# Kernel tuning notes

Measured on AMD Instinct MI355X. Metric: run time of the kernel, lower is better.

Reference implementation:

```python
import jax, jax.numpy as jnp
import numpy as np

B, S, D = 2, 2048, 1024
H, HD = 16, 64  # num_heads, head_dim
EPS = 1e-6      # flax LayerNorm default
ROPE_BASE = 10000.0


def _layernorm(x, scale, bias=None, eps=EPS):
    mu = jnp.mean(x, axis=-1, keepdims=True)
    var = jnp.mean(jnp.square(x - mu), axis=-1, keepdims=True)
    y = (x - mu) * jax.lax.rsqrt(var + eps) * scale
    return y + bias if bias is not None else y


def _rotate_half(x):
    x1, x2 = x[..., : x.shape[-1] // 2], x[..., x.shape[-1] // 2 :]
    return jnp.concatenate((-x2, x1), axis=-1)


def _rope_tables(seq_len, head_dim, dtype):
    inv_freq = 1.0 / ROPE_BASE ** (jnp.arange(0, head_dim, 2, dtype=jnp.float32) / head_dim)
    t = jnp.arange(seq_len, dtype=jnp.float32)
    freqs = jnp.einsum('i,j->ij', t, inv_freq)          # [S, HD/2]
    emb = jnp.concatenate((freqs, freqs), axis=-1)      # [S, HD]
    return jnp.cos(emb).astype(dtype), jnp.sin(emb).astype(dtype)


def setup_inputs() -> dict:
    key = jax.random.key(0)
    ks = jax.random.split(key, 4)
    return {
        'x': jax.random.normal(ks[0], (B, S, D), dtype=jnp.float32),
        'w_qkv': jax.random.normal(ks[1], (D, 3 * D), dtype=jnp.float32) * (1.0 / np.sqrt(D)),
        'b_qkv': jnp.zeros((3 * D,), dtype=jnp.float32),
        'w_out': jax.random.normal(ks[2], (D, D), dtype=jnp.float32) * (0.1 / np.sqrt(D)),
        'b_out': jnp.zeros((D,), dtype=jnp.float32),
        'ln_scale': jnp.ones((D,), dtype=jnp.float32),
        'ln_bias': jnp.zeros((D,), dtype=jnp.float32),
        'q_scale': jnp.ones((HD,), dtype=jnp.float32),
        'k_scale': jnp.ones((HD,), dtype=jnp.float32),
    }


def reference(x, w_qkv, b_qkv, w_out, b_out, ln_scale, ln_bias, q_scale, k_scale):
    b, s, d = x.shape
    # input LayerNorm
    xn = _layernorm(x, ln_scale, ln_bias)
    # fused QKV projection
    qkv = xn @ w_qkv + b_qkv                              # [B, S, 3D]
    q, k, v = jnp.split(qkv, 3, axis=-1)
    def to_bhsd(t):
        return t.reshape(b, s, H, HD).transpose(0, 2, 1, 3)
    q, k, v = to_bhsd(q), to_bhsd(k), to_bhsd(v)          # [B, H, S, HD]
    # per-head QK LayerNorm (no bias)
    q = _layernorm(q, q_scale)
    k = _layernorm(k, k_scale)
    # RoPE
    cos, sin = _rope_tables(s, HD, q.dtype)               # [S, HD]
    cos, sin = cos[None, None], sin[None, None]
    q = q * cos + _rotate_half(q) * sin
    k = k * cos + _rotate_half(k) * sin
    # scaled dot-product attention (softmax over key positions)
    scale = 1.0 / np.sqrt(HD)
    scores = jnp.einsum('bhqd,bhkd->bhqk', q, k) * scale  # [B, H, S, S]
    probs = jax.nn.softmax(scores, axis=-1)
    attn = jnp.einsum('bhqk,bhkd->bhqd', probs, v)        # [B, H, S, HD]
    attn = attn.transpose(0, 2, 1, 3).reshape(b, s, d)
    return attn @ w_out + b_out
```

## Files before the change

kernel.cpp:

```cpp
#include <hip/hip_runtime.h>
#include <math.h>

#define BB 2
#define SS 2048
#define DD 1024
#define HH 16
#define HDD 64
static constexpr float EPS = 1e-6f;

typedef __bf16 bf16x8 __attribute__((ext_vector_type(8)));
typedef __bf16 bf16x4 __attribute__((ext_vector_type(4)));
typedef float f32x4 __attribute__((ext_vector_type(4)));
typedef __attribute__((address_space(1))) const unsigned int gas_u32;
typedef __attribute__((address_space(3))) unsigned int las_u32;

__device__ __forceinline__ unsigned short f2bf(float f) {
    unsigned int u = __float_as_uint(f);
    u = (u + 0x7FFFu + ((u >> 16) & 1u)) >> 16;
    return (unsigned short)u;
}

__device__ __forceinline__ uint2 pack4bf(float a, float b, float c, float d) {
    bf16x4 v;
    v[0] = (__bf16)a; v[1] = (__bf16)b; v[2] = (__bf16)c; v[3] = (__bf16)d;
    return *(uint2*)&v;
}

__device__ __forceinline__ void async_ld16(const unsigned short* g, unsigned short* l) {
    __builtin_amdgcn_global_load_lds((gas_u32*)g, (las_u32*)l, 16, 0, 0);
}

__global__ __launch_bounds__(256) void cast_transpose(const float* __restrict__ w,
                                                      unsigned short* __restrict__ wt,
                                                      int K, int N) {
    __shared__ float tile[32][36];
    const int n0 = blockIdx.x * 32;
    const int k0 = blockIdx.y * 32;
    const int t = threadIdx.x;
    const int r = t >> 3;
    const int c = (t & 7) * 4;
    *(float4*)&tile[r][c] = *(const float4*)(w + (size_t)(k0 + r) * N + n0 + c);
    __syncthreads();
    unsigned short o[4];
#pragma unroll
    for (int i = 0; i < 4; i++) o[i] = f2bf(tile[c + i][r]);
    *(uint2*)(wt + (size_t)(n0 + r) * K + k0 + c) = *(uint2*)o;
}

__global__ __launch_bounds__(256) void rope_tables(float* __restrict__ ctab,
                                                   float* __restrict__ stab) {
    const int idx = blockIdx.x * 256 + threadIdx.x;
    const int s = idx >> 5;
    const int i = idx & 31;
    const float ang = (float)s * exp2f(-(float)i * (13.287712379549449f / 32.f));
    ctab[idx] = cosf(ang);
    stab[idx] = sinf(ang);
}

__global__ __launch_bounds__(256) void ln_kernel(const float* __restrict__ x,
                                                 const float* __restrict__ scale,
                                                 const float* __restrict__ bias,
                                                 unsigned short* __restrict__ xn) {
    __shared__ float red[4];
    const int row = blockIdx.x;
    const int t = threadIdx.x;
    const float* xr = x + (size_t)row * DD + t * 4;

    float4 v = *(const float4*)xr;
    float s = v.x + v.y + v.z + v.w;
#pragma unroll
    for (int o = 32; o; o >>= 1) s += __shfl_xor(s, o);
    if ((t & 63) == 0) red[t >> 6] = s;
    __syncthreads();
    const float mu = (red[0] + red[1] + red[2] + red[3]) * (1.f / DD);

    float4 d = {v.x - mu, v.y - mu, v.z - mu, v.w - mu};
    float sq = d.x * d.x + d.y * d.y + d.z * d.z + d.w * d.w;
#pragma unroll
    for (int o = 32; o; o >>= 1) sq += __shfl_xor(sq, o);
    __syncthreads();
    if ((t & 63) == 0) red[t >> 6] = sq;
    __syncthreads();
    const float var = (red[0] + red[1] + red[2] + red[3]) * (1.f / DD);
    const float rstd = rsqrtf(var + EPS);

    const float4 sc = *(const float4*)(scale + t * 4);
    const float4 bi = *(const float4*)(bias + t * 4);
    unsigned short o[4];
    o[0] = f2bf(d.x * rstd * sc.x + bi.x);
    o[1] = f2bf(d.y * rstd * sc.y + bi.y);
    o[2] = f2bf(d.z * rstd * sc.z + bi.z);
    o[3] = f2bf(d.w * rstd * sc.w + bi.w);
    *(uint2*)(xn + (size_t)row * DD + t * 4) = *(uint2*)o;
}

__global__ __launch_bounds__(256) void gemm_mfma_bt(const unsigned short* __restrict__ A,
                                                    const unsigned short* __restrict__ Bt,
                                                    const float* __restrict__ bias,
                                                    float* __restrict__ C,
                                                    int M, int N, int K) {
    __shared__ __align__(16) unsigned short As[128][32];
    __shared__ __align__(16) unsigned short Bs[128][32];

    const int bm = blockIdx.y * 128;
    const int bn = blockIdx.x * 128;
    const int t = threadIdx.x;
    const int wv = t >> 6;
    const int ln = t & 63;
    const int m16 = ln & 15;
    const int quad = ln >> 4;
    const int wm = (wv >> 1) * 64;
    const int wn = (wv & 1) * 64;

    f32x4 acc[4][4];
#pragma unroll
    for (int i = 0; i < 4; i++)
#pragma unroll
        for (int j = 0; j < 4; j++) acc[i][j] = (f32x4){0.f, 0.f, 0.f, 0.f};

    const int srow = wv * 32 + (ln >> 2);
    const int sk = (ln & 3) * 8;
    const unsigned short* aptr = A + (size_t)(bm + srow) * K + sk;
    const unsigned short* bptr = Bt + (size_t)(bn + srow) * K + sk;
    unsigned short* al0 = &As[wv * 32][0];
    unsigned short* al1 = &As[wv * 32 + 16][0];
    unsigned short* bl0 = &Bs[wv * 32][0];
    unsigned short* bl1 = &Bs[wv * 32 + 16][0];

    for (int k0 = 0; k0 < K; k0 += 32) {
        __syncthreads();
        async_ld16(aptr, al0);
        async_ld16(aptr + 16 * (size_t)K, al1);
        async_ld16(bptr, bl0);
        async_ld16(bptr + 16 * (size_t)K, bl1);
        __syncthreads();

        bf16x8 af[4], bf[4];
#pragma unroll
        for (int i = 0; i < 4; i++)
            af[i] = *(const bf16x8*)&As[wm + i * 16 + m16][quad * 8];
#pragma unroll
        for (int j = 0; j < 4; j++)
            bf[j] = *(const bf16x8*)&Bs[wn + j * 16 + m16][quad * 8];
#pragma unroll
        for (int i = 0; i < 4; i++)
#pragma unroll
            for (int j = 0; j < 4; j++)
                acc[i][j] = __builtin_amdgcn_mfma_f32_16x16x32_bf16(af[i], bf[j], acc[i][j], 0, 0, 0);

        aptr += 32;
        bptr += 32;
    }

#pragma unroll
    for (int j = 0; j < 4; j++) {
        const int n = bn + wn + j * 16 + m16;
        const float bv = bias[n];
#pragma unroll
        for (int i = 0; i < 4; i++) {
            float* cp = C + (size_t)(bm + wm + i * 16 + quad * 4) * N + n;
#pragma unroll
            for (int r = 0; r < 4; r++)
                cp[(size_t)r * N] = acc[i][j][r] + bv;
        }
    }
}

__global__ __launch_bounds__(256) void gemm_qkv_fused(const unsigned short* __restrict__ A,
                                                      const unsigned short* __restrict__ Bt,
                                                      const float* __restrict__ bias,
                                                      const float* __restrict__ q_scale,
                                                      const float* __restrict__ k_scale,
                                                      const float* __restrict__ ctab,
                                                      const float* __restrict__ stab,
                                                      unsigned short* __restrict__ qt,
                                                      unsigned short* __restrict__ kt,
                                                      unsigned short* __restrict__ vt,
                                                      int K) {
    __shared__ __align__(16) unsigned short As[128][32];
    __shared__ __align__(16) unsigned short Bs[128][32];

    const int bm = blockIdx.y * 128;
    const int bn = blockIdx.x * 128;
    const int t = threadIdx.x;
    const int wv = t >> 6;
    const int ln = t & 63;
    const int m16 = ln & 15;
    const int quad = ln >> 4;
    const int wm = (wv >> 1) * 64;
    const int wn = (wv & 1) * 64;

    f32x4 acc[4][4];
#pragma unroll
    for (int i = 0; i < 4; i++)
#pragma unroll
        for (int j = 0; j < 4; j++) acc[i][j] = (f32x4){0.f, 0.f, 0.f, 0.f};

    const int srow = wv * 32 + (ln >> 2);
    const int sk = (ln & 3) * 8;
    const unsigned short* aptr = A + (size_t)(bm + srow) * K + sk;
    const unsigned short* bptr = Bt + (size_t)(bn + srow) * K + sk;
    unsigned short* al0 = &As[wv * 32][0];
    unsigned short* al1 = &As[wv * 32 + 16][0];
    unsigned short* bl0 = &Bs[wv * 32][0];
    unsigned short* bl1 = &Bs[wv * 32 + 16][0];

    for (int k0 = 0; k0 < K; k0 += 32) {
        __syncthreads();
        async_ld16(aptr, al0);
        async_ld16(aptr + 16 * (size_t)K, al1);
        async_ld16(bptr, bl0);
        async_ld16(bptr + 16 * (size_t)K, bl1);
        __syncthreads();

        bf16x8 af[4], bf[4];
#pragma unroll
        for (int i = 0; i < 4; i++)
            af[i] = *(const bf16x8*)&As[wm + i * 16 + m16][quad * 8];
#pragma unroll
        for (int j = 0; j < 4; j++)
            bf[j] = *(const bf16x8*)&Bs[wn + j * 16 + m16][quad * 8];
#pragma unroll
        for (int i = 0; i < 4; i++)
#pragma unroll
            for (int j = 0; j < 4; j++)
                acc[i][j] = __builtin_amdgcn_mfma_f32_16x16x32_bf16(af[i], bf[j], acc[i][j], 0, 0, 0);

        aptr += 32;
        bptr += 32;
    }

    const int type = bn >> 10;
    const int h = ((bn & 1023) + wn) >> 6;
    const int rowbase = bm + wm;

    if (type == 2) {
        float bv[4];
#pragma unroll
        for (int j = 0; j < 4; j++) bv[j] = bias[bn + wn + j * 16 + m16];
#pragma unroll
        for (int i = 0; i < 4; i++) {
#pragma unroll
            for (int r = 0; r < 4; r++) {
                const int R = rowbase + i * 16 + quad * 4 + r;
                const int b_ = R >> 11;
                const int s_ = R & (SS - 1);
                unsigned short* orow =
                    vt + (((size_t)(b_ * HH + h) * SS) + s_) * HDD + m16;
#pragma unroll
                for (int j = 0; j < 4; j++)
                    orow[j * 16] = f2bf(acc[i][j][r] + bv[j]);
            }
        }
    } else {
        const float* scalp = (type == 0) ? q_scale : k_scale;
        const float outscale = (type == 0) ? 0.18033688011112042f : 1.0f;
        unsigned short* dst = (type == 0) ? qt : kt;
        float scl[4], bv[4];
#pragma unroll
        for (int j = 0; j < 4; j++) {
            scl[j] = scalp[j * 16 + m16];
            bv[j] = bias[bn + wn + j * 16 + m16];
        }
#pragma unroll
        for (int i = 0; i < 4; i++) {
#pragma unroll
            for (int r = 0; r < 4; r++) {
                const int R = rowbase + i * 16 + quad * 4 + r;
                const int b_ = R >> 11;
                const int s_ = R & (SS - 1);
                float v0 = acc[i][0][r] + bv[0];
                float v1 = acc[i][1][r] + bv[1];
                float v2 = acc[i][2][r] + bv[2];
                float v3 = acc[i][3][r] + bv[3];
                float sm = v0 + v1 + v2 + v3;
                sm += __shfl_xor(sm, 1);
                sm += __shfl_xor(sm, 2);
                sm += __shfl_xor(sm, 4);
                sm += __shfl_xor(sm, 8);
                const float mu = sm * (1.f / 64.f);
                v0 -= mu; v1 -= mu; v2 -= mu; v3 -= mu;
                float sq = v0 * v0 + v1 * v1 + v2 * v2 + v3 * v3;
                sq += __shfl_xor(sq, 1);
                sq += __shfl_xor(sq, 2);
                sq += __shfl_xor(sq, 4);
                sq += __shfl_xor(sq, 8);
                const float rstd = rsqrtf(sq * (1.f / 64.f) + EPS);
                v0 *= rstd * scl[0];
                v1 *= rstd * scl[1];
                v2 *= rstd * scl[2];
                v3 *= rstd * scl[3];
                const float c0 = ctab[s_ * 32 + m16];
                const float s0 = stab[s_ * 32 + m16];
                const float c1 = ctab[s_ * 32 + 16 + m16];
                const float s1 = stab[s_ * 32 + 16 + m16];
                const float o0 = (v0 * c0 - v2 * s0) * outscale;
                const float o1 = (v1 * c1 - v3 * s1) * outscale;
                const float o2 = (v2 * c0 + v0 * s0) * outscale;
                const float o3 = (v3 * c1 + v1 * s1) * outscale;
                unsigned short* orow =
                    dst + (((size_t)(b_ * HH + h) * SS) + s_) * HDD + m16;
                orow[0]  = f2bf(o0);
                orow[16] = f2bf(o1);
                orow[32] = f2bf(o2);
                orow[48] = f2bf(o3);
            }
        }
    }
}

__global__ __launch_bounds__(256) void transpose_v(const unsigned short* __restrict__ vt,
                                                   unsigned short* __restrict__ vtT) {
    __shared__ unsigned short tile[64][72];
    const int bh = blockIdx.x >> 5;
    const int s0 = (blockIdx.x & 31) * 64;
    const int t = threadIdx.x;
    const int row = t >> 2;
    const int c0 = (t & 3) * 16;
    const unsigned short* src = vt + ((size_t)bh * SS + s0 + row) * HDD + c0;
    *(uint4*)&tile[row][c0]     = *(const uint4*)(src);
    *(uint4*)&tile[row][c0 + 8] = *(const uint4*)(src + 8);
    __syncthreads();
    unsigned short outv[16];
#pragma unroll
    for (int i = 0; i < 16; i++) outv[i] = tile[c0 + i][row];
    unsigned short* dst = vtT + ((size_t)bh * HDD + row) * SS + s0 + c0;
    *(uint4*)dst       = *(uint4*)&outv[0];
    *(uint4*)(dst + 8) = *(uint4*)&outv[8];
}

__global__ __launch_bounds__(256, 4) void attn_mfma(const unsigned short* __restrict__ qt,
                                                    const unsigned short* __restrict__ kt,
                                                    const unsigned short* __restrict__ vtT,
                                                    unsigned short* __restrict__ attn) {
    __shared__ __align__(16) unsigned short KsS[64 * 64];
    __shared__ __align__(16) unsigned short VsS[64 * 64];
    __shared__ __align__(16) unsigned short PbS[4][16 * 64];

    const int bid = blockIdx.x;
    const int swz = (bid & 7) * 128 + (bid >> 3);
    const int bh = swz >> 5;
    const int q0 = (swz & 31) * 64;
    const int t = threadIdx.x;
    const int wq = t >> 6;
    const int lane = t & 63;
    const int m16 = lane & 15;
    const int quad = lane >> 4;
    const int m7 = m16 & 7;

    const int cs = quad ^ m7;
    const int koff = m16 * 64 + cs * 8;
    const int srow = t >> 2;
    const int sch = (t & 3) * 2;
    const int sw0 = srow * 64 + ((sch)     ^ (srow & 7)) * 8;
    const int sw1 = srow * 64 + ((sch + 1) ^ (srow & 7)) * 8;
    const int pwb = m16 * 64 + 4 * (quad & 1);
    const int qh = quad >> 1;

    bf16x8 qb[2];
    {
        const unsigned short* qp =
            qt + ((size_t)bh * SS + q0 + wq * 16 + m16) * HDD + quad * 8;
        qb[0] = *(const bf16x8*)qp;
        qb[1] = *(const bf16x8*)(qp + 32);
    }

    bf16x8 ones;
#pragma unroll
    for (int j = 0; j < 8; j++) ones[j] = (__bf16)1.0f;

    f32x4 O[4];
#pragma unroll
    for (int f = 0; f < 4; f++) O[f] = (f32x4){0.f, 0.f, 0.f, 0.f};
    f32x4 lacc = (f32x4){0.f, 0.f, 0.f, 0.f};

    const unsigned short* kbase = kt + (size_t)bh * SS * HDD;
    const unsigned short* vbase = vtT + (size_t)bh * HDD * SS;
    const f32x4 cinit = (f32x4){-12.f, -12.f, -12.f, -12.f};

    uint4 kr0, kr1, vr0, vr1;
    {
        const unsigned short* ksrc = kbase + (size_t)srow * HDD + sch * 8;
        const unsigned short* vsrc = vbase + (size_t)srow * SS + sch * 8;
        kr0 = *(const uint4*)ksrc;
        kr1 = *(const uint4*)(ksrc + 8);
        vr0 = *(const uint4*)vsrc;
        vr1 = *(const uint4*)(vsrc + 8);
    }

    for (int k0 = 0; k0 < SS; k0 += 64) {
        __syncthreads();
        *(uint4*)&KsS[sw0] = kr0;
        *(uint4*)&KsS[sw1] = kr1;
        *(uint4*)&VsS[sw0] = vr0;
        *(uint4*)&VsS[sw1] = vr1;
        __syncthreads();

        f32x4 S[4];
        __builtin_amdgcn_s_setprio(1);
#pragma unroll
        for (int g = 0; g < 4; g++) {
            const bf16x8 ka0 = *(const bf16x8*)&KsS[g * 1024 + koff];
            const bf16x8 ka1 = *(const bf16x8*)&KsS[g * 1024 + (koff ^ 32)];
            f32x4 a = __builtin_amdgcn_mfma_f32_16x16x32_bf16(ka0, qb[0], cinit, 0, 0, 0);
            a = __builtin_amdgcn_mfma_f32_16x16x32_bf16(ka1, qb[1], a, 0, 0, 0);
            S[g] = a;
        }
        __builtin_amdgcn_s_setprio(0);

#pragma unroll
        for (int g = 0; g < 4; g++) {
            const float p0 = exp2f(S[g][0]);
            const float p1 = exp2f(S[g][1]);
            const float p2 = exp2f(S[g][2]);
            const float p3 = exp2f(S[g][3]);
            *(uint2*)&PbS[wq][pwb + ((2 * g + qh) ^ m7) * 8] =
                pack4bf(p0, p1, p2, p3);
        }

        if (k0 + 64 < SS) {
            const unsigned short* ksrc = kbase + (size_t)(k0 + 64 + srow) * HDD + sch * 8;
            const unsigned short* vsrc = vbase + (size_t)srow * SS + (k0 + 64) + sch * 8;
            kr0 = *(const uint4*)ksrc;
            kr1 = *(const uint4*)(ksrc + 8);
            vr0 = *(const uint4*)vsrc;
            vr1 = *(const uint4*)(vsrc + 8);
        }

        asm volatile("s_waitcnt lgkmcnt(0)" ::: "memory");

        bf16x8 pb[2];
        pb[0] = *(const bf16x8*)&PbS[wq][koff];
        pb[1] = *(const bf16x8*)&PbS[wq][koff ^ 32];

        __builtin_amdgcn_s_setprio(1);
        lacc = __builtin_amdgcn_mfma_f32_16x16x32_bf16(ones, pb[0], lacc, 0, 0, 0);
        lacc = __builtin_amdgcn_mfma_f32_16x16x32_bf16(ones, pb[1], lacc, 0, 0, 0);
#pragma unroll
        for (int f = 0; f < 4; f++) {
            const bf16x8 va0 = *(const bf16x8*)&VsS[f * 1024 + koff];
            const bf16x8 va1 = *(const bf16x8*)&VsS[f * 1024 + (koff ^ 32)];
            O[f] = __builtin_amdgcn_mfma_f32_16x16x32_bf16(va0, pb[0], O[f], 0, 0, 0);
            O[f] = __builtin_amdgcn_mfma_f32_16x16x32_bf16(va1, pb[1], O[f], 0, 0, 0);
        }
        __builtin_amdgcn_s_setprio(0);
    }

    const int b_ = bh >> 4;
    const int h_ = bh & 15;
    {
        const float inv = 1.f / lacc[0];
        const int s_ = q0 + wq * 16 + m16;
        unsigned short* orow = attn + ((size_t)b_ * SS + s_) * DD + h_ * HDD;
#pragma unroll
        for (int f = 0; f < 4; f++)
            *(uint2*)(orow + f * 16 + quad * 4) =
                pack4bf(O[f][0] * inv, O[f][1] * inv,
                        O[f][2] * inv, O[f][3] * inv);
    }
}

extern "C" void kernel_launch(void* const* d_in, const int* in_sizes, int n_in,
                              void* d_out, int out_size, void* d_ws, size_t ws_size,
                              hipStream_t stream) {
    const float* x        = (const float*)d_in[0];
    const float* w_qkv    = (const float*)d_in[1];
    const float* b_qkv    = (const float*)d_in[2];
    const float* w_out    = (const float*)d_in[3];
    const float* b_out    = (const float*)d_in[4];
    const float* ln_scale = (const float*)d_in[5];
    const float* ln_bias  = (const float*)d_in[6];
    const float* q_scale  = (const float*)d_in[7];
    const float* k_scale  = (const float*)d_in[8];
    float* out = (float*)d_out;

    char* ws = (char*)d_ws;
    const size_t MB = 1024 * 1024;
    unsigned short* xn    = (unsigned short*)(ws + 0);
    float*          ctab  = (float*)(ws + 9 * MB);
    float*          stab  = (float*)(ws + 10 * MB);
    unsigned short* wqkvT = (unsigned short*)(ws + 64 * MB);
    unsigned short* woutT = (unsigned short*)(ws + 70 * MB);
    unsigned short* qt    = (unsigned short*)(ws + 72 * MB);
    unsigned short* kt    = (unsigned short*)(ws + 80 * MB);
    unsigned short* vt    = (unsigned short*)(ws + 88 * MB);
    unsigned short* vtT   = (unsigned short*)(ws + 96 * MB);
    unsigned short* attn  = (unsigned short*)(ws + 104 * MB);

    const int M = BB * SS;

    cast_transpose<<<dim3(3 * DD / 32, DD / 32), 256, 0, stream>>>(w_qkv, wqkvT, DD, 3 * DD);
    cast_transpose<<<dim3(DD / 32, DD / 32), 256, 0, stream>>>(w_out, woutT, DD, DD);
    rope_tables<<<SS * 32 / 256, 256, 0, stream>>>(ctab, stab);

    ln_kernel<<<M, 256, 0, stream>>>(x, ln_scale, ln_bias, xn);

    gemm_qkv_fused<<<dim3(3 * DD / 128, M / 128), 256, 0, stream>>>(
        xn, wqkvT, b_qkv, q_scale, k_scale, ctab, stab, qt, kt, vt, DD);

    transpose_v<<<BB * HH * (SS / 64), 256, 0, stream>>>(vt, vtT);

    attn_mfma<<<dim3(BB * HH * (SS / 64)), 256, 0, stream>>>(qt, kt, vtT, attn);

    gemm_mfma_bt<<<dim3(DD / 128, M / 128), 256, 0, stream>>>(attn, woutT, b_out, out,
                                                              M, DD, DD);
}
```

Before: 240.4 us.

## Split attention over key halves with combine pass; shrink output GEMM tile

Attention now splits each (batch, head, query-tile) across two blocks that each process half of the keys. Partial normalized outputs and row sums go to workspace, and a new combine kernel merges them. This doubles the grid from 1024 to 2048 blocks to fill more CUs, at the cost of an extra kernel launch and extra memory traffic for the partials. The combine relies on a fixed softmax offset (no running max), so a plain sum-weighted merge is valid. The output projection GEMM also switches to 64x128 tiles so it launches more blocks.

Result: no change. 242.0 us (+0.7%).

```diff
diff --git a/kernel.cpp b/kernel.cpp
--- a/kernel.cpp
+++ b/kernel.cpp
@@ -18,6 +18,10 @@
     unsigned int u = __float_as_uint(f);
     u = (u + 0x7FFFu + ((u >> 16) & 1u)) >> 16;
     return (unsigned short)u;
+}
+
+__device__ __forceinline__ float b2f(unsigned short u) {
+    return __uint_as_float((unsigned int)u << 16);
 }
 
 __device__ __forceinline__ uint2 pack4bf(float a, float b, float c, float d) {
@@ -94,71 +98,70 @@
     *(uint2*)(xn + (size_t)row * DD + t * 4) = *(uint2*)o;
 }
 
-__global__ __launch_bounds__(256) void gemm_mfma_bt(const unsigned short* __restrict__ A,
-                                                    const unsigned short* __restrict__ Bt,
-                                                    const float* __restrict__ bias,
-                                                    float* __restrict__ C,
-                                                    int M, int N, int K) {
-    __shared__ __align__(16) unsigned short As[128][32];
+__global__ __launch_bounds__(256) void gemm_out_64(const unsigned short* __restrict__ A,
+                                                   const unsigned short* __restrict__ Bt,
+                                                   const float* __restrict__ bias,
+                                                   float* __restrict__ C,
+                                                   int M, int N, int K) {
+    __shared__ __align__(16) unsigned short As[64][32];
     __shared__ __align__(16) unsigned short Bs[128][32];
 
-    const int bm = blockIdx.y * 128;
+    const int bm = blockIdx.y * 64;
     const int bn = blockIdx.x * 128;
     const int t = threadIdx.x;
     const int wv = t >> 6;
     const int ln = t & 63;
     const int m16 = ln & 15;
     const int quad = ln >> 4;
-    const int wm = (wv >> 1) * 64;
-    const int wn = (wv & 1) * 64;
-
-    f32x4 acc[4][4];
+    const int wn = wv * 32;
+
+    f32x4 acc[4][2];
 #pragma unroll
     for (int i = 0; i < 4; i++)
 #pragma unroll
-        for (int j = 0; j < 4; j++) acc[i][j] = (f32x4){0.f, 0.f, 0.f, 0.f};
-
-    const int srow = wv * 32 + (ln >> 2);
+        for (int j = 0; j < 2; j++) acc[i][j] = (f32x4){0.f, 0.f, 0.f, 0.f};
+
+    const int srow = ln >> 2;
     const int sk = (ln & 3) * 8;
-    const unsigned short* aptr = A + (size_t)(bm + srow) * K + sk;
-    const unsigned short* bptr = Bt + (size_t)(bn + srow) * K + sk;
-    unsigned short* al0 = &As[wv * 32][0];
-    unsigned short* al1 = &As[wv * 32 + 16][0];
+    const unsigned short* aptr = A + (size_t)(bm + wv * 16 + srow) * K + sk;
+    const unsigned short* bptr0 = Bt + (size_t)(bn + wv * 32 + srow) * K + sk;
+    const unsigned short* bptr1 = Bt + (size_t)(bn + wv * 32 + 16 + srow) * K + sk;
+    unsigned short* al = &As[wv * 16][0];
     unsigned short* bl0 = &Bs[wv * 32][0];
     unsigned short* bl1 = &Bs[wv * 32 + 16][0];
 
     for (int k0 = 0; k0 < K; k0 += 32) {
         __syncthreads();
-        async_ld16(aptr, al0);
-        async_ld16(aptr + 16 * (size_t)K, al1);
-        async_ld16(bptr, bl0);
-        async_ld16(bptr + 16 * (size_t)K, bl1);
+        async_ld16(aptr, al);
+        async_ld16(bptr0, bl0);
+        async_ld16(bptr1, bl1);
         __syncthreads();
 
-        bf16x8 af[4], bf[4];
+        bf16x8 af[4], bf[2];
 #pragma unroll
         for (int i = 0; i < 4; i++)
-            af[i] = *(const bf16x8*)&As[wm + i * 16 + m16][quad * 8];
-#pragma unroll
-        for (int j = 0; j < 4; j++)
+            af[i] = *(const bf16x8*)&As[i * 16 + m16][quad * 8];
+#pragma unroll
+        for (int j = 0; j < 2; j++)
             bf[j] = *(const bf16x8*)&Bs[wn + j * 16 + m16][quad * 8];
 #pragma unroll
         for (int i = 0; i < 4; i++)
 #pragma unroll
-            for (int j = 0; j < 4; j++)
+            for (int j = 0; j < 2; j++)
                 acc[i][j] = __builtin_amdgcn_mfma_f32_16x16x32_bf16(af[i], bf[j], acc[i][j], 0, 0, 0);
 
         aptr += 32;
-        bptr += 32;
-    }
-
-#pragma unroll
-    for (int j = 0; j < 4; j++) {
+        bptr0 += 32;
+        bptr1 += 32;
+    }
+
+#pragma unroll
+    for (int j = 0; j < 2; j++) {
         const int n = bn + wn + j * 16 + m16;
         const float bv = bias[n];
 #pragma unroll
         for (int i = 0; i < 4; i++) {
-            float* cp = C + (size_t)(bm + wm + i * 16 + quad * 4) * N + n;
+            float* cp = C + (size_t)(bm + i * 16 + quad * 4) * N + n;
 #pragma unroll
             for (int r = 0; r < 4; r++)
                 cp[(size_t)r * N] = acc[i][j][r] + bv;
@@ -332,15 +335,17 @@
 __global__ __launch_bounds__(256, 4) void attn_mfma(const unsigned short* __restrict__ qt,
                                                     const unsigned short* __restrict__ kt,
                                                     const unsigned short* __restrict__ vtT,
-                                                    unsigned short* __restrict__ attn) {
+                                                    unsigned short* __restrict__ Opart,
+                                                    float* __restrict__ lpart) {
     __shared__ __align__(16) unsigned short KsS[64 * 64];
     __shared__ __align__(16) unsigned short VsS[64 * 64];
     __shared__ __align__(16) unsigned short PbS[4][16 * 64];
 
     const int bid = blockIdx.x;
-    const int swz = (bid & 7) * 128 + (bid >> 3);
-    const int bh = swz >> 5;
-    const int q0 = (swz & 31) * 64;
+    const int swz = (bid & 7) * 256 + (bid >> 3);
+    const int bh = swz >> 6;
+    const int q0 = ((swz >> 1) & 31) * 64;
+    const int ks = swz & 1;
     const int t = threadIdx.x;
     const int wq = t >> 6;
     const int lane = t & 63;
@@ -378,17 +383,20 @@
     const unsigned short* vbase = vtT + (size_t)bh * HDD * SS;
     const f32x4 cinit = (f32x4){-12.f, -12.f, -12.f, -12.f};
 
+    const int kstart = ks * (SS / 2);
+    const int kend = kstart + SS / 2;
+
     uint4 kr0, kr1, vr0, vr1;
     {
-        const unsigned short* ksrc = kbase + (size_t)srow * HDD + sch * 8;
-        const unsigned short* vsrc = vbase + (size_t)srow * SS + sch * 8;
+        const unsigned short* ksrc = kbase + (size_t)(kstart + srow) * HDD + sch * 8;
+        const unsigned short* vsrc = vbase + (size_t)srow * SS + kstart + sch * 8;
         kr0 = *(const uint4*)ksrc;
         kr1 = *(const uint4*)(ksrc + 8);
         vr0 = *(const uint4*)vsrc;
         vr1 = *(const uint4*)(vsrc + 8);
     }
 
-    for (int k0 = 0; k0 < SS; k0 += 64) {
+    for (int k0 = kstart; k0 < kend; k0 += 64) {
         __syncthreads();
         *(uint4*)&KsS[sw0] = kr0;
         *(uint4*)&KsS[sw1] = kr1;
@@ -418,7 +426,7 @@
                 pack4bf(p0, p1, p2, p3);
         }
 
-        if (k0 + 64 < SS) {
+        if (k0 + 64 < kend) {
             const unsigned short* ksrc = kbase + (size_t)(k0 + 64 + srow) * HDD + sch * 8;
             const unsigned short* vsrc = vbase + (size_t)srow * SS + (k0 + 64) + sch * 8;
             kr0 = *(const uint4*)ksrc;
@@ -451,13 +459,45 @@
     {
         const float inv = 1.f / lacc[0];
         const int s_ = q0 + wq * 16 + m16;
-        unsigned short* orow = attn + ((size_t)b_ * SS + s_) * DD + h_ * HDD;
+        unsigned short* orow = Opart + (size_t)ks * ((size_t)BB * SS * DD) +
+                               ((size_t)b_ * SS + s_) * DD + h_ * HDD;
 #pragma unroll
         for (int f = 0; f < 4; f++)
             *(uint2*)(orow + f * 16 + quad * 4) =
                 pack4bf(O[f][0] * inv, O[f][1] * inv,
                         O[f][2] * inv, O[f][3] * inv);
-    }
+        if (quad == 0)
+            lpart[ks * (32 * SS) + bh * SS + s_] = lacc[0];
+    }
+}
+
+__global__ __launch_bounds__(256) void combine_attn(const unsigned short* __restrict__ Opart,
+                                                    const float* __restrict__ lpart,
+                                                    unsigned short* __restrict__ attn) {
+    const int row = blockIdx.x;
+    const int t = threadIdx.x;
+    const int c = t * 4;
+    const int h = t >> 4;
+    const int b = row >> 11;
+    const int s = row & (SS - 1);
+
+    const size_t off = (size_t)row * DD + c;
+    const uint2 u0 = *(const uint2*)(Opart + off);
+    const uint2 u1 = *(const uint2*)(Opart + (size_t)BB * SS * DD + off);
+    const unsigned short* p0 = (const unsigned short*)&u0;
+    const unsigned short* p1 = (const unsigned short*)&u1;
+
+    const int li = (b * HH + h) * SS + s;
+    const float l0 = lpart[li];
+    const float l1 = lpart[32 * SS + li];
+    const float w = 1.f / (l0 + l1);
+    const float w0 = l0 * w;
+    const float w1 = l1 * w;
+
+    *(uint2*)(attn + off) = pack4bf(w0 * b2f(p0[0]) + w1 * b2f(p1[0]),
+                                    w0 * b2f(p0[1]) + w1 * b2f(p1[1]),
+                                    w0 * b2f(p0[2]) + w1 * b2f(p1[2]),
+                                    w0 * b2f(p0[3]) + w1 * b2f(p1[3]));
 }
 
 extern "C" void kernel_launch(void* const* d_in, const int* in_sizes, int n_in,
@@ -477,8 +517,10 @@
     char* ws = (char*)d_ws;
     const size_t MB = 1024 * 1024;
     unsigned short* xn    = (unsigned short*)(ws + 0);
+    float*          lpart = (float*)(ws + 8 * MB);
     float*          ctab  = (float*)(ws + 9 * MB);
     float*          stab  = (float*)(ws + 10 * MB);
+    unsigned short* Opart = (unsigned short*)(ws + 16 * MB);
     unsigned short* wqkvT = (unsigned short*)(ws + 64 * MB);
     unsigned short* woutT = (unsigned short*)(ws + 70 * MB);
     unsigned short* qt    = (unsigned short*)(ws + 72 * MB);
@@ -500,8 +542,10 @@
 
     transpose_v<<<BB * HH * (SS / 64), 256, 0, stream>>>(vt, vtT);
 
-    attn_mfma<<<dim3(BB * HH * (SS / 64)), 256, 0, stream>>>(qt, kt, vtT, attn);
-
-    gemm_mfma_bt<<<dim3(DD / 128, M / 128), 256, 0, stream>>>(attn, woutT, b_out, out,
-                                                              M, DD, DD);
-}
+    attn_mfma<<<dim3(2 * BB * HH * (SS / 64)), 256, 0, stream>>>(qt, kt, vtT, Opart, lpart);
+
+    combine_attn<<<M, 256, 0, stream>>>(Opart, lpart, attn);
+
+    gemm_out_64<<<dim3(DD / 128, M / 64), 256, 0, stream>>>(attn, woutT, b_out, out,
+                                                            M, DD, DD);
+}
```
